# Performance work log

Measured on AMD Instinct MI355X. Metric: run time of the kernel, lower is better.

Reference implementation:

```python
import jax, jax.numpy as jnp
import numpy as np

T, H, I, E, K = 2048, 1024, 768, 16, 4

def setup_inputs() -> dict:
    key = jax.random.key(0)
    k1, k2, k3, k4, k5 = jax.random.split(key, 5)
    hidden_states = jax.random.normal(k1, (T, H), dtype=jnp.float32)
    top_k_index = jax.random.randint(k2, (T, K), 0, E, dtype=jnp.int64)
    top_k_weights = jax.random.uniform(k3, (T, K), dtype=jnp.float32)
    gate_up_proj = jax.random.normal(k4, (E, 2 * I, H), dtype=jnp.float32) * 0.02
    down_proj = jax.random.normal(k5, (E, H, I), dtype=jnp.float32) * 0.02
    return {"hidden_states": hidden_states, "top_k_index": top_k_index,
            "top_k_weights": top_k_weights, "gate_up_proj": gate_up_proj,
            "down_proj": down_proj}

def reference(hidden_states, top_k_index, top_k_weights, gate_up_proj, down_proj):
    # Masked dense MoE: scan over experts, each expert does full-token GEMMs
    # and a per-token combine weight (sum of routing weights where routed to e).
    # index_add over token_idx == sum over k of (mask * weight) * expert_out.
    n_experts = gate_up_proj.shape[0]

    def body(acc, xs):
        w_gu, w_d, e = xs  # [2I,H], [H,I], scalar
        gu = hidden_states @ w_gu.T                 # [T, 2I]
        gate, up = jnp.split(gu, 2, axis=-1)        # [T, I] each
        h = jax.nn.silu(gate) * up                  # [T, I]
        out = h @ w_d.T                             # [T, H]
        w_tok = jnp.sum(jnp.where(top_k_index == e, top_k_weights, 0.0), axis=-1)  # [T]
        return acc + out * w_tok[:, None], None

    acc0 = jnp.zeros_like(hidden_states)
    final, _ = jax.lax.scan(body, acc0, (gate_up_proj, down_proj, jnp.arange(n_experts)))
    return final
```

## Files before the change

kernel.cpp:

```cpp
#include <hip/hip_runtime.h>
#include <hip/hip_bf16.h>
#include <stdint.h>

#define T_TOK 2048
#define H_DIM 1024
#define I_DIM 768
#define E_NUM 16
#define K_TOP 4
#define NSLOT (T_TOK * K_TOP)
#define PSLOT 10240
#define NTILE 80

typedef short  s16x8 __attribute__((ext_vector_type(8)));
typedef float  f32x4 __attribute__((ext_vector_type(4)));
typedef unsigned short u16x8 __attribute__((ext_vector_type(8)));

__device__ __forceinline__ void gload16(const void* g, void* l) {
  __builtin_amdgcn_global_load_lds(
      (const __attribute__((address_space(1))) uint32_t*)g,
      (__attribute__((address_space(3))) uint32_t*)l, 16, 0, 0);
}

__device__ __forceinline__ unsigned short f2bf(float f) {
  __hip_bfloat16 h = __float2bfloat16(f);
  return *reinterpret_cast<unsigned short*>(&h);
}

__device__ __forceinline__ void write_b_row(char* bregion, int r, int half,
                                            f32x4 f0, f32x4 f1, f32x4 f2, f32x4 f3) {
  u16x8 c0, c1;
  c0[0]=f2bf(f0[0]); c0[1]=f2bf(f0[1]); c0[2]=f2bf(f0[2]); c0[3]=f2bf(f0[3]);
  c0[4]=f2bf(f1[0]); c0[5]=f2bf(f1[1]); c0[6]=f2bf(f1[2]); c0[7]=f2bf(f1[3]);
  c1[0]=f2bf(f2[0]); c1[1]=f2bf(f2[1]); c1[2]=f2bf(f2[2]); c1[3]=f2bf(f2[3]);
  c1[4]=f2bf(f3[0]); c1[5]=f2bf(f3[1]); c1[6]=f2bf(f3[2]); c1[7]=f2bf(f3[3]);
  int xr = (r >> 1) & 3;
  char* wb = bregion + r * 64;
  *(u16x8*)(wb + (((2*half + 0) ^ xr) * 16)) = c0;
  *(u16x8*)(wb + (((2*half + 1) ^ xr) * 16)) = c1;
}

__global__ __launch_bounds__(256) void cvt_bf16_kernel(
    const float* __restrict__ in, unsigned short* __restrict__ out, int n8) {
  int i = blockIdx.x * 256 + threadIdx.x;
  if (i >= n8) return;
  const float4* p = (const float4*)in;
  float4 a = p[2 * (size_t)i];
  float4 b = p[2 * (size_t)i + 1];
  u16x8 o;
  o[0] = f2bf(a.x); o[1] = f2bf(a.y); o[2] = f2bf(a.z); o[3] = f2bf(a.w);
  o[4] = f2bf(b.x); o[5] = f2bf(b.y); o[6] = f2bf(b.z); o[7] = f2bf(b.w);
  *(u16x8*)(out + (size_t)i * 8) = o;
}

__global__ __launch_bounds__(256) void route_kernel(
    const int* __restrict__ idx, const float* __restrict__ wts,
    int* __restrict__ slot_tok, float* __restrict__ slot_w,
    int* __restrict__ slot_of, int* __restrict__ tile_expert) {
  __shared__ int cnt[256][16];
  __shared__ int tot[16];
  __shared__ int pb[17];
  int tid = threadIdx.x;

  for (int e = 0; e < 16; ++e) cnt[tid][e] = 0;
  const int s0 = tid * 32;
  for (int i = 0; i < 32; ++i) {
    int e = idx[s0 + i] & 15;
    cnt[tid][e]++;
  }
  __syncthreads();
  if (tid < 16) {
    int run = 0;
    for (int c = 0; c < 256; ++c) { int v = cnt[c][tid]; cnt[c][tid] = run; run += v; }
    tot[tid] = run;
  }
  __syncthreads();
  if (tid == 0) {
    int acc = 0;
    for (int e = 0; e < 16; ++e) { pb[e] = acc; acc += (tot[e] + 127) & ~127; }
    pb[16] = acc;
  }
  __syncthreads();
  for (int p = tid; p < PSLOT; p += 256) { slot_tok[p] = 0; slot_w[p] = 0.0f; }
  if (tid < NTILE) {
    int ef = -1;
    for (int e = 0; e < 16; ++e)
      if (tid * 128 >= pb[e] && tid * 128 < pb[e + 1]) ef = e;
    tile_expert[tid] = ef;
  }
  __syncthreads();
  for (int i = 0; i < 32; ++i) {
    int s = s0 + i;
    int e = idx[s] & 15;
    int pos = pb[e] + cnt[tid][e]++;
    slot_tok[pos] = s >> 2;
    slot_w[pos]   = wts[s];
    slot_of[s]    = pos;
  }
}

__global__ __launch_bounds__(256) void gemm1_kernel(
    const unsigned short* __restrict__ Xbf,
    const float* __restrict__ Wgu,
    const int* __restrict__ slot_tok,
    const int* __restrict__ tile_expert,
    unsigned short* __restrict__ hbuf) {
  int e = tile_expert[blockIdx.y];
  if (e < 0) return;
  int bx = blockIdx.x;
  int m0 = blockIdx.y * 128;
  int tid = threadIdx.x;
  int lane = tid & 63, w = tid >> 6;
  int wr = w >> 1, wc = w & 1;

  __shared__ short lds[2 * 8192];
  char* buf0 = (char*)lds;
  char* buf1 = buf0 + 16384;

  int srow = tid >> 2;
  int swzc = ((tid & 3) ^ ((tid >> 3) & 3)) * 16;
  int tok0 = slot_tok[m0 + srow];
  int tok1 = slot_tok[m0 + 64 + srow];
  const char* gA0 = (const char*)(Xbf + (size_t)tok0 * H_DIM) + swzc;
  const char* gA1 = (const char*)(Xbf + (size_t)tok1 * H_DIM) + swzc;

  int brow = tid >> 1;
  int half = tid & 1;
  int prow = (brow < 64) ? (bx * 64 + brow) : (768 + bx * 64 + (brow - 64));
  const float* gB = Wgu + ((size_t)e * 1536 + prow) * H_DIM + half * 16;

  int pswz = ((lane >> 4) ^ (((lane & 15) >> 1) & 3)) * 8;

  f32x4 accg[4][2] = {};
  f32x4 accu[4][2] = {};
  f32x4 ra0, ra1, ra2, ra3, rb0, rb1, rb2, rb3;

#define G1_STAGE(bufp, r0, r1, r2, r3, kt) do {               \
    int ko_ = (kt) * 64;                                      \
    gload16(gA0 + ko_, (bufp) + tid * 16);                    \
    gload16(gA1 + ko_, (bufp) + 4096 + tid * 16);             \
    const f32x4* p_ = (const f32x4*)(gB + (size_t)(kt) * 32); \
    r0 = p_[0]; r1 = p_[1]; r2 = p_[2]; r3 = p_[3];           \
  } while (0)

#define G1_COMPUTE(bufp) do {                                                          \
    const short* La = (const short*)(bufp);                                            \
    s16x8 af[4], bgf[2], buf2[2];                                                      \
    _Pragma("unroll")                                                                  \
    for (int mi = 0; mi < 4; ++mi)                                                     \
      af[mi] = *(const s16x8*)(La + (wr * 64 + mi * 16 + (lane & 15)) * 32 + pswz);    \
    _Pragma("unroll")                                                                  \
    for (int ni = 0; ni < 2; ++ni) {                                                   \
      int row = wc * 32 + ni * 16 + (lane & 15);                                       \
      bgf[ni]  = *(const s16x8*)(La + 4096 + row * 32 + pswz);                         \
      buf2[ni] = *(const s16x8*)(La + 6144 + row * 32 + pswz);                         \
    }                                                                                  \
    _Pragma("unroll")                                                                  \
    for (int mi = 0; mi < 4; ++mi)                                                     \
      _Pragma("unroll")                                                                \
      for (int ni = 0; ni < 2; ++ni) {                                                 \
        accg[mi][ni] = __builtin_amdgcn_mfma_f32_16x16x32_bf16(af[mi], bgf[ni],  accg[mi][ni], 0, 0, 0); \
        accu[mi][ni] = __builtin_amdgcn_mfma_f32_16x16x32_bf16(af[mi], buf2[ni], accu[mi][ni], 0, 0, 0); \
      }                                                                                \
  } while (0)

  G1_STAGE(buf0, ra0, ra1, ra2, ra3, 0);
  for (int kt = 0; kt < 32; kt += 2) {
    G1_STAGE(buf1, rb0, rb1, rb2, rb3, kt + 1);
    asm volatile("s_waitcnt vmcnt(6)" ::: "memory");
    write_b_row(buf0 + 8192, brow, half, ra0, ra1, ra2, ra3);
    asm volatile("s_waitcnt lgkmcnt(0)" ::: "memory");
    __builtin_amdgcn_s_barrier();
    G1_COMPUTE(buf0);
    __builtin_amdgcn_s_barrier();
    if (kt + 2 < 32) {
      G1_STAGE(buf0, ra0, ra1, ra2, ra3, kt + 2);
      asm volatile("s_waitcnt vmcnt(6)" ::: "memory");
    } else {
      asm volatile("s_waitcnt vmcnt(0)" ::: "memory");
    }
    write_b_row(buf1 + 8192, brow, half, rb0, rb1, rb2, rb3);
    asm volatile("s_waitcnt lgkmcnt(0)" ::: "memory");
    __builtin_amdgcn_s_barrier();
    G1_COMPUTE(buf1);
    __builtin_amdgcn_s_barrier();
  }
#undef G1_STAGE
#undef G1_COMPUTE

#pragma unroll
  for (int mi = 0; mi < 4; ++mi) {
#pragma unroll
    for (int ni = 0; ni < 2; ++ni) {
      int col = bx * 64 + wc * 32 + ni * 16 + (lane & 15);
#pragma unroll
      for (int q = 0; q < 4; ++q) {
        int m = m0 + wr * 64 + mi * 16 + (lane >> 4) * 4 + q;
        float g = accg[mi][ni][q];
        float u = accu[mi][ni][q];
        float s = g / (1.0f + __expf(-g));
        hbuf[(size_t)m * I_DIM + col] = f2bf(s * u);
      }
    }
  }
}

__global__ __launch_bounds__(256) void gemm2_kernel(
    const unsigned short* __restrict__ hbuf,
    const float* __restrict__ Wd,
    const int* __restrict__ slot_tok,
    const float* __restrict__ slot_w,
    const int* __restrict__ tile_expert,
    float* __restrict__ y) {
  int e = tile_expert[blockIdx.y];
  if (e < 0) return;
  int bx = blockIdx.x;
  int m0 = blockIdx.y * 128;
  int tid = threadIdx.x;
  int lane = tid & 63, w = tid >> 6;
  int wr = w >> 1, wc = w & 1;

  __shared__ short lds[2 * 8192];
  char* buf0 = (char*)lds;
  char* buf1 = buf0 + 16384;

  int srow = tid >> 2;
  int swzc = ((tid & 3) ^ ((tid >> 3) & 3)) * 16;
  const char* gA0 = (const char*)(hbuf + (size_t)(m0 + srow) * I_DIM) + swzc;
  const char* gA1 = (const char*)(hbuf + (size_t)(m0 + 64 + srow) * I_DIM) + swzc;

  int brow = tid >> 1;
  int half = tid & 1;
  const float* gB = Wd + ((size_t)e * 1024 + bx * 128 + brow) * I_DIM + half * 16;

  int pswz = ((lane >> 4) ^ (((lane & 15) >> 1) & 3)) * 8;

  f32x4 acc[4][4] = {};
  f32x4 ra0, ra1, ra2, ra3, rb0, rb1, rb2, rb3;

#define G2_STAGE(bufp, r0, r1, r2, r3, kt) do {               \
    int ko_ = (kt) * 64;                                      \
    gload16(gA0 + ko_, (bufp) + tid * 16);                    \
    gload16(gA1 + ko_, (bufp) + 4096 + tid * 16);             \
    const f32x4* p_ = (const f32x4*)(gB + (size_t)(kt) * 32); \
    r0 = p_[0]; r1 = p_[1]; r2 = p_[2]; r3 = p_[3];           \
  } while (0)

#define G2_COMPUTE(bufp) do {                                                          \
    const short* La = (const short*)(bufp);                                            \
    s16x8 af[4], bf[4];                                                                \
    _Pragma("unroll")                                                                  \
    for (int mi = 0; mi < 4; ++mi)                                                     \
      af[mi] = *(const s16x8*)(La + (wr * 64 + mi * 16 + (lane & 15)) * 32 + pswz);    \
    _Pragma("unroll")                                                                  \
    for (int ni = 0; ni < 4; ++ni)                                                     \
      bf[ni] = *(const s16x8*)(La + 4096 + (wc * 64 + ni * 16 + (lane & 15)) * 32 + pswz); \
    _Pragma("unroll")                                                                  \
    for (int mi = 0; mi < 4; ++mi)                                                     \
      _Pragma("unroll")                                                                \
      for (int ni = 0; ni < 4; ++ni)                                                   \
        acc[mi][ni] = __builtin_amdgcn_mfma_f32_16x16x32_bf16(af[mi], bf[ni], acc[mi][ni], 0, 0, 0); \
  } while (0)

  G2_STAGE(buf0, ra0, ra1, ra2, ra3, 0);
  for (int kt = 0; kt < 24; kt += 2) {
    G2_STAGE(buf1, rb0, rb1, rb2, rb3, kt + 1);
    asm volatile("s_waitcnt vmcnt(6)" ::: "memory");
    write_b_row(buf0 + 8192, brow, half, ra0, ra1, ra2, ra3);
    asm volatile("s_waitcnt lgkmcnt(0)" ::: "memory");
    __builtin_amdgcn_s_barrier();
    G2_COMPUTE(buf0);
    __builtin_amdgcn_s_barrier();
    if (kt + 2 < 24) {
      G2_STAGE(buf0, ra0, ra1, ra2, ra3, kt + 2);
      asm volatile("s_waitcnt vmcnt(6)" ::: "memory");
    } else {
      asm volatile("s_waitcnt vmcnt(0)" ::: "memory");
    }
    write_b_row(buf1 + 8192, brow, half, rb0, rb1, rb2, rb3);
    asm volatile("s_waitcnt lgkmcnt(0)" ::: "memory");
    __builtin_amdgcn_s_barrier();
    G2_COMPUTE(buf1);
    __builtin_amdgcn_s_barrier();
  }
#undef G2_STAGE
#undef G2_COMPUTE

#pragma unroll
  for (int mi = 0; mi < 4; ++mi) {
#pragma unroll
    for (int q = 0; q < 4; ++q) {
      int m = m0 + wr * 64 + mi * 16 + (lane >> 4) * 4 + q;
      float wgt = slot_w[m];
      float* orow = y + (size_t)m * H_DIM + bx * 128 + wc * 64 + (lane & 15);
#pragma unroll
      for (int ni = 0; ni < 4; ++ni)
        orow[ni * 16] = acc[mi][ni][q] * wgt;
    }
  }
}

__global__ __launch_bounds__(256) void combine_kernel(
    const float* __restrict__ y, const int* __restrict__ slot_of,
    float* __restrict__ out) {
  int t = blockIdx.x;
  int c = threadIdx.x * 4;
  int s0 = slot_of[t * 4 + 0], s1 = slot_of[t * 4 + 1];
  int s2 = slot_of[t * 4 + 2], s3 = slot_of[t * 4 + 3];
  f32x4 v0 = *(const f32x4*)(y + (size_t)s0 * H_DIM + c);
  f32x4 v1 = *(const f32x4*)(y + (size_t)s1 * H_DIM + c);
  f32x4 v2 = *(const f32x4*)(y + (size_t)s2 * H_DIM + c);
  f32x4 v3 = *(const f32x4*)(y + (size_t)s3 * H_DIM + c);
  f32x4 r = (v0 + v1) + (v2 + v3);
  *(f32x4*)(out + (size_t)t * H_DIM + c) = r;
}

extern "C" void kernel_launch(void* const* d_in, const int* in_sizes, int n_in,
                              void* d_out, int out_size, void* d_ws, size_t ws_size,
                              hipStream_t stream) {
  const float* hs       = (const float*)d_in[0];
  const int*   topk_idx = (const int*)d_in[1];
  const float* topk_w   = (const float*)d_in[2];
  const float* w_gu     = (const float*)d_in[3];
  const float* w_d      = (const float*)d_in[4];
  float* out = (float*)d_out;

  char* ws = (char*)d_ws;
  unsigned short* Xbf  = (unsigned short*)(ws);
  unsigned short* hbuf = (unsigned short*)(ws + 4194304);
  float*          y    = (float*)(ws + 19922944);
  int*   slot_tok    = (int*)(ws + 61865984);
  float* slot_w      = (float*)(ws + 61906944);
  int*   slot_of     = (int*)(ws + 61947904);
  int*   tile_expert = (int*)(ws + 61980672);

  cvt_bf16_kernel<<<1024, 256, 0, stream>>>(hs, Xbf, T_TOK * H_DIM / 8);
  route_kernel<<<1, 256, 0, stream>>>(topk_idx, topk_w, slot_tok, slot_w, slot_of, tile_expert);

  gemm1_kernel<<<dim3(12, NTILE), 256, 0, stream>>>(Xbf, w_gu, slot_tok, tile_expert, hbuf);
  gemm2_kernel<<<dim3(8, NTILE), 256, 0, stream>>>(hbuf, w_d, slot_tok, slot_w, tile_expert, y);
  combine_kernel<<<T_TOK, 256, 0, stream>>>(y, slot_of, out);
}
```

Measured before the change: 145.2 us.

## Deepen fp32 weight prefetch to three stages and remap blocks across XCDs

Both expert GEMM kernels now keep three register stages of fp32 weight loads in flight, up from one, in a 4-way unrolled loop. Each iteration writes the converted bf16 B tile for the next step while computing on the current buffer, with one barrier pair per k-step. This hides more global-load latency on the weight stream. Block IDs are also remapped with an XCD-style swizzle (bid&7 stride) so neighbouring tiles that share an expert or rows land on the same XCD, which should improve L2 reuse. The costs are higher register pressure and clamped redundant tail loads.

```diff
diff --git a/kernel.cpp b/kernel.cpp
--- a/kernel.cpp
+++ b/kernel.cpp
@@ -14,6 +14,8 @@
 typedef short  s16x8 __attribute__((ext_vector_type(8)));
 typedef float  f32x4 __attribute__((ext_vector_type(4)));
 typedef unsigned short u16x8 __attribute__((ext_vector_type(8)));
+
+#define MEMFENCE asm volatile("" ::: "memory")
 
 __device__ __forceinline__ void gload16(const void* g, void* l) {
   __builtin_amdgcn_global_load_lds(
@@ -98,16 +100,20 @@
   }
 }
 
+
 __global__ __launch_bounds__(256) void gemm1_kernel(
     const unsigned short* __restrict__ Xbf,
     const float* __restrict__ Wgu,
     const int* __restrict__ slot_tok,
     const int* __restrict__ tile_expert,
     unsigned short* __restrict__ hbuf) {
-  int e = tile_expert[blockIdx.y];
+  int bid  = blockIdx.y * 12 + blockIdx.x;
+  int sbid = (bid & 7) * 120 + (bid >> 3);
+  int by   = sbid / 12;
+  int bx   = sbid % 12;
+  int e = tile_expert[by];
   if (e < 0) return;
-  int bx = blockIdx.x;
-  int m0 = blockIdx.y * 128;
+  int m0 = by * 128;
   int tid = threadIdx.x;
   int lane = tid & 63, w = tid >> 6;
   int wr = w >> 1, wc = w & 1;
@@ -132,14 +138,20 @@
 
   f32x4 accg[4][2] = {};
   f32x4 accu[4][2] = {};
-  f32x4 ra0, ra1, ra2, ra3, rb0, rb1, rb2, rb3;
-
-#define G1_STAGE(bufp, r0, r1, r2, r3, kt) do {               \
-    int ko_ = (kt) * 64;                                      \
+  f32x4 s0_0, s0_1, s0_2, s0_3, s1_0, s1_1, s1_2, s1_3;
+  f32x4 s2_0, s2_1, s2_2, s2_3, s3_0, s3_1, s3_2, s3_3;
+
+#define NT1 32
+#define A_GLOAD1(kt, bufp) do {                               \
+    int kk_ = (kt) < NT1 ? (kt) : NT1 - 1;                    \
+    int ko_ = kk_ * 64;                                       \
     gload16(gA0 + ko_, (bufp) + tid * 16);                    \
     gload16(gA1 + ko_, (bufp) + 4096 + tid * 16);             \
-    const f32x4* p_ = (const f32x4*)(gB + (size_t)(kt) * 32); \
-    r0 = p_[0]; r1 = p_[1]; r2 = p_[2]; r3 = p_[3];           \
+  } while (0)
+#define B_LOAD1(v0, v1, v2, v3, kt) do {                      \
+    int kk_ = (kt) < NT1 ? (kt) : NT1 - 1;                    \
+    const f32x4* p_ = (const f32x4*)(gB + (size_t)kk_ * 32);  \
+    v0 = p_[0]; v1 = p_[1]; v2 = p_[2]; v3 = p_[3];           \
   } while (0)
 
 #define G1_COMPUTE(bufp) do {                                                          \
@@ -163,29 +175,43 @@
       }                                                                                \
   } while (0)
 
-  G1_STAGE(buf0, ra0, ra1, ra2, ra3, 0);
-  for (int kt = 0; kt < 32; kt += 2) {
-    G1_STAGE(buf1, rb0, rb1, rb2, rb3, kt + 1);
-    asm volatile("s_waitcnt vmcnt(6)" ::: "memory");
-    write_b_row(buf0 + 8192, brow, half, ra0, ra1, ra2, ra3);
-    asm volatile("s_waitcnt lgkmcnt(0)" ::: "memory");
-    __builtin_amdgcn_s_barrier();
-    G1_COMPUTE(buf0);
-    __builtin_amdgcn_s_barrier();
-    if (kt + 2 < 32) {
-      G1_STAGE(buf0, ra0, ra1, ra2, ra3, kt + 2);
-      asm volatile("s_waitcnt vmcnt(6)" ::: "memory");
-    } else {
-      asm volatile("s_waitcnt vmcnt(0)" ::: "memory");
-    }
-    write_b_row(buf1 + 8192, brow, half, rb0, rb1, rb2, rb3);
-    asm volatile("s_waitcnt lgkmcnt(0)" ::: "memory");
-    __builtin_amdgcn_s_barrier();
-    G1_COMPUTE(buf1);
-    __builtin_amdgcn_s_barrier();
-  }
-#undef G1_STAGE
+#define ITER1(kt, wv0, wv1, wv2, wv3, lv0, lv1, lv2, lv3) do {  \
+    char* cbuf_ = ((kt) & 1) ? buf1 : buf0;                     \
+    char* nbuf_ = ((kt) & 1) ? buf0 : buf1;                     \
+    MEMFENCE;                                                   \
+    A_GLOAD1((kt) + 1, nbuf_);                                  \
+    MEMFENCE;                                                   \
+    B_LOAD1(lv0, lv1, lv2, lv3, (kt) + 3);                      \
+    asm volatile("s_waitcnt vmcnt(10)" ::: "memory");           \
+    write_b_row(nbuf_ + 8192, brow, half, wv0, wv1, wv2, wv3);  \
+    asm volatile("s_waitcnt lgkmcnt(0)" ::: "memory");          \
+    __builtin_amdgcn_s_barrier();                               \
+    MEMFENCE;                                                   \
+    G1_COMPUTE(cbuf_);                                          \
+    MEMFENCE;                                                   \
+    __builtin_amdgcn_s_barrier();                               \
+  } while (0)
+
+  A_GLOAD1(0, buf0);
+  MEMFENCE;
+  B_LOAD1(s0_0, s0_1, s0_2, s0_3, 0);
+  MEMFENCE;
+  B_LOAD1(s1_0, s1_1, s1_2, s1_3, 1);
+  MEMFENCE;
+  B_LOAD1(s2_0, s2_1, s2_2, s2_3, 2);
+  asm volatile("s_waitcnt vmcnt(8)" ::: "memory");
+  write_b_row(buf0 + 8192, brow, half, s0_0, s0_1, s0_2, s0_3);
+
+  for (int kt = 0; kt < NT1; kt += 4) {
+    ITER1(kt + 0, s1_0, s1_1, s1_2, s1_3, s3_0, s3_1, s3_2, s3_3);
+    ITER1(kt + 1, s2_0, s2_1, s2_2, s2_3, s0_0, s0_1, s0_2, s0_3);
+    ITER1(kt + 2, s3_0, s3_1, s3_2, s3_3, s1_0, s1_1, s1_2, s1_3);
+    ITER1(kt + 3, s0_0, s0_1, s0_2, s0_3, s2_0, s2_1, s2_2, s2_3);
+  }
+#undef ITER1
 #undef G1_COMPUTE
+#undef B_LOAD1
+#undef A_GLOAD1
 
 #pragma unroll
   for (int mi = 0; mi < 4; ++mi) {
@@ -211,10 +237,13 @@
     const float* __restrict__ slot_w,
     const int* __restrict__ tile_expert,
     float* __restrict__ y) {
-  int e = tile_expert[blockIdx.y];
+  int bid  = blockIdx.y * 8 + blockIdx.x;
+  int sbid = (bid & 7) * 80 + (bid >> 3);
+  int by   = sbid >> 3;
+  int bx   = sbid & 7;
+  int e = tile_expert[by];
   if (e < 0) return;
-  int bx = blockIdx.x;
-  int m0 = blockIdx.y * 128;
+  int m0 = by * 128;
   int tid = threadIdx.x;
   int lane = tid & 63, w = tid >> 6;
   int wr = w >> 1, wc = w & 1;
@@ -235,14 +264,20 @@
   int pswz = ((lane >> 4) ^ (((lane & 15) >> 1) & 3)) * 8;
 
   f32x4 acc[4][4] = {};
-  f32x4 ra0, ra1, ra2, ra3, rb0, rb1, rb2, rb3;
-
-#define G2_STAGE(bufp, r0, r1, r2, r3, kt) do {               \
-    int ko_ = (kt) * 64;                                      \
+  f32x4 s0_0, s0_1, s0_2, s0_3, s1_0, s1_1, s1_2, s1_3;
+  f32x4 s2_0, s2_1, s2_2, s2_3, s3_0, s3_1, s3_2, s3_3;
+
+#define NT2 24
+#define A_GLOAD2(kt, bufp) do {                               \
+    int kk_ = (kt) < NT2 ? (kt) : NT2 - 1;                    \
+    int ko_ = kk_ * 64;                                       \
     gload16(gA0 + ko_, (bufp) + tid * 16);                    \
     gload16(gA1 + ko_, (bufp) + 4096 + tid * 16);             \
-    const f32x4* p_ = (const f32x4*)(gB + (size_t)(kt) * 32); \
-    r0 = p_[0]; r1 = p_[1]; r2 = p_[2]; r3 = p_[3];           \
+  } while (0)
+#define B_LOAD2(v0, v1, v2, v3, kt) do {                      \
+    int kk_ = (kt) < NT2 ? (kt) : NT2 - 1;                    \
+    const f32x4* p_ = (const f32x4*)(gB + (size_t)kk_ * 32);  \
+    v0 = p_[0]; v1 = p_[1]; v2 = p_[2]; v3 = p_[3];           \
   } while (0)
 
 #define G2_COMPUTE(bufp) do {                                                          \
@@ -261,29 +296,43 @@
         acc[mi][ni] = __builtin_amdgcn_mfma_f32_16x16x32_bf16(af[mi], bf[ni], acc[mi][ni], 0, 0, 0); \
   } while (0)
 
-  G2_STAGE(buf0, ra0, ra1, ra2, ra3, 0);
-  for (int kt = 0; kt < 24; kt += 2) {
-    G2_STAGE(buf1, rb0, rb1, rb2, rb3, kt + 1);
-    asm volatile("s_waitcnt vmcnt(6)" ::: "memory");
-    write_b_row(buf0 + 8192, brow, half, ra0, ra1, ra2, ra3);
-    asm volatile("s_waitcnt lgkmcnt(0)" ::: "memory");
-    __builtin_amdgcn_s_barrier();
-    G2_COMPUTE(buf0);
-    __builtin_amdgcn_s_barrier();
-    if (kt + 2 < 24) {
-      G2_STAGE(buf0, ra0, ra1, ra2, ra3, kt + 2);
-      asm volatile("s_waitcnt vmcnt(6)" ::: "memory");
-    } else {
-      asm volatile("s_waitcnt vmcnt(0)" ::: "memory");
-    }
-    write_b_row(buf1 + 8192, brow, half, rb0, rb1, rb2, rb3);
-    asm volatile("s_waitcnt lgkmcnt(0)" ::: "memory");
-    __builtin_amdgcn_s_barrier();
-    G2_COMPUTE(buf1);
-    __builtin_amdgcn_s_barrier();
-  }
-#undef G2_STAGE
+#define ITER2(kt, wv0, wv1, wv2, wv3, lv0, lv1, lv2, lv3) do {  \
+    char* cbuf_ = ((kt) & 1) ? buf1 : buf0;                     \
+    char* nbuf_ = ((kt) & 1) ? buf0 : buf1;                     \
+    MEMFENCE;                                                   \
+    A_GLOAD2((kt) + 1, nbuf_);                                  \
+    MEMFENCE;                                                   \
+    B_LOAD2(lv0, lv1, lv2, lv3, (kt) + 3);                      \
+    asm volatile("s_waitcnt vmcnt(10)" ::: "memory");           \
+    write_b_row(nbuf_ + 8192, brow, half, wv0, wv1, wv2, wv3);  \
+    asm volatile("s_waitcnt lgkmcnt(0)" ::: "memory");          \
+    __builtin_amdgcn_s_barrier();                               \
+    MEMFENCE;                                                   \
+    G2_COMPUTE(cbuf_);                                          \
+    MEMFENCE;                                                   \
+    __builtin_amdgcn_s_barrier();                               \
+  } while (0)
+
+  A_GLOAD2(0, buf0);
+  MEMFENCE;
+  B_LOAD2(s0_0, s0_1, s0_2, s0_3, 0);
+  MEMFENCE;
+  B_LOAD2(s1_0, s1_1, s1_2, s1_3, 1);
+  MEMFENCE;
+  B_LOAD2(s2_0, s2_1, s2_2, s2_3, 2);
+  asm volatile("s_waitcnt vmcnt(8)" ::: "memory");
+  write_b_row(buf0 + 8192, brow, half, s0_0, s0_1, s0_2, s0_3);
+
+  for (int kt = 0; kt < NT2; kt += 4) {
+    ITER2(kt + 0, s1_0, s1_1, s1_2, s1_3, s3_0, s3_1, s3_2, s3_3);
+    ITER2(kt + 1, s2_0, s2_1, s2_2, s2_3, s0_0, s0_1, s0_2, s0_3);
+    ITER2(kt + 2, s3_0, s3_1, s3_2, s3_3, s1_0, s1_1, s1_2, s1_3);
+    ITER2(kt + 3, s0_0, s0_1, s0_2, s0_3, s2_0, s2_1, s2_2, s2_3);
+  }
+#undef ITER2
 #undef G2_COMPUTE
+#undef B_LOAD2
+#undef A_GLOAD2
 
 #pragma unroll
   for (int mi = 0; mi < 4; ++mi) {
```

Measured after the change: 135.4 us. 6.7% less time.
